# Performance work log

Measured on AMD Instinct MI355X. Metric: run time of the kernel, lower is better.

The kernel has to match this reference:

```python
import jax, jax.numpy as jnp
import numpy as np

N_NODES = 100000   # number of graph nodes (users + items)
N_EDGES = 1600000  # nonzeros of the normalized adjacency (avg degree 16)
D_FEAT = 48        # node embedding dimension


def setup_inputs() -> dict:
    key = jax.random.key(0)
    k_t, k_x, k_r, k_c, k_v = jax.random.split(key, 5)
    t = jax.random.normal(k_t, (1,), dtype=jnp.float32)
    x = jax.random.normal(k_x, (N_NODES, D_FEAT), dtype=jnp.float32)
    # COO sparse adjacency: rows sorted (CSR-like ordering), random cols,
    # positive edge weights mimicking symmetric-normalized adjacency values.
    rows = jnp.sort(jax.random.randint(k_r, (N_EDGES,), 0, N_NODES, dtype=jnp.int32))
    cols = jax.random.randint(k_c, (N_EDGES,), 0, N_NODES, dtype=jnp.int32)
    vals = jax.random.uniform(k_v, (N_EDGES,), dtype=jnp.float32)
    return {"t": t, "x": x, "rows": rows, "cols": cols, "vals": vals}


def reference(t, x, rows, cols, vals):
    # torch.sparse.mm(graph, x): for each nonzero (r, c, v), out[r] += v * x[c].
    # t (ODE time) is unused by the module's forward.
    msgs = x[cols] * vals[:, None]                      # [E, D] gathered, scaled messages
    out = jax.ops.segment_sum(msgs, rows, num_segments=N_NODES)  # scatter-add to rows
    return out
```

## Files before the change

### kernel.cpp

```cpp
#include <hip/hip_runtime.h>
#include <hip/hip_bf16.h>
#include <hip/hip_fp16.h>


#define D_FEAT 48
#define TPR 12
#define RPB 16
#define BLOCK (TPR * RPB)
#define ROW_BYTES 64

typedef float vfloat4 __attribute__((ext_vector_type(4)));

__global__ void build_row_ptr_scatter(const int* __restrict__ rows,
                                      int* __restrict__ row_ptr,
                                      int n_edges, int n_nodes) {
    int e = blockIdx.x * blockDim.x + threadIdx.x;
    if (e >= n_edges) return;
    const int r     = rows[e];
    const int rprev = (e == 0) ? -1 : rows[e - 1];
    for (int q = rprev + 1; q <= r; ++q) row_ptr[q] = e;
    if (e == n_edges - 1) {
        for (int q = r + 1; q <= n_nodes; ++q) row_ptr[q] = n_edges;
    }
}

__global__ __launch_bounds__(BLOCK) void convert_x_i8(
        const float* __restrict__ x,
        unsigned char* __restrict__ xq, int n_nodes) {
    __shared__ float smax[RPB][TPR];
    const int tid = threadIdx.x;
    const int fg  = tid % TPR;
    const int rib = tid / TPR;
    const int r   = blockIdx.x * RPB + rib;

    float4 f = make_float4(0.f, 0.f, 0.f, 0.f);
    if (r < n_nodes)
        f = reinterpret_cast<const float4*>(x)[(size_t)r * (D_FEAT / 4) + fg];

    float lmax = fmaxf(fmaxf(fabsf(f.x), fabsf(f.y)),
                       fmaxf(fabsf(f.z), fabsf(f.w)));
    smax[rib][fg] = lmax;
    __syncthreads();

    float rmax = 0.f;
#pragma unroll
    for (int i = 0; i < TPR; ++i) rmax = fmaxf(rmax, smax[rib][i]);
    if (r >= n_nodes) return;

    const float scale = rmax * (1.0f / 127.0f);
    const float inv   = (rmax > 0.f) ? (127.0f / rmax) : 0.f;

    union { signed char c[4]; unsigned int u; } pk;
    pk.c[0] = (signed char)(int)rintf(fminf(fmaxf(f.x * inv, -127.f), 127.f));
    pk.c[1] = (signed char)(int)rintf(fminf(fmaxf(f.y * inv, -127.f), 127.f));
    pk.c[2] = (signed char)(int)rintf(fminf(fmaxf(f.z * inv, -127.f), 127.f));
    pk.c[3] = (signed char)(int)rintf(fminf(fmaxf(f.w * inv, -127.f), 127.f));

    unsigned char* row = xq + (size_t)r * ROW_BYTES;
    *reinterpret_cast<unsigned int*>(row + fg * 4) = pk.u;
    if (fg == 0) *reinterpret_cast<float*>(row + 48) = scale;
}

__device__ __forceinline__ void fma4_q(vfloat4& acc, float vs, unsigned int q) {
    acc.x += vs * (float)(int)(signed char)(q & 0xffu);
    acc.y += vs * (float)(int)(signed char)((q >> 8) & 0xffu);
    acc.z += vs * (float)(int)(signed char)((q >> 16) & 0xffu);
    acc.w += vs * (float)(int)(signed char)(q >> 24);
}

__global__ __launch_bounds__(BLOCK) void spmm_rows_i8(
        const int* __restrict__ row_ptr,
        const int* __restrict__ cols,
        const float* __restrict__ vals,
        const unsigned char* __restrict__ xq,
        float* __restrict__ out,
        int n_nodes) {
    const int tid = threadIdx.x;
    const int fg  = tid % TPR;
    const int rib = tid / TPR;
    const int r   = blockIdx.x * RPB + rib;
    if (r >= n_nodes) return;

    const int e0 = row_ptr[r];
    const int e1 = row_ptr[r + 1];

    vfloat4 acc = (vfloat4)(0.f);

    int e = e0;
    for (; e + 7 < e1; e += 8) {
        int   c[8];
        float v[8];
#pragma unroll
        for (int j = 0; j < 8; ++j) { c[j] = cols[e + j]; v[j] = vals[e + j]; }
        unsigned int q[8];
        float        s[8];
#pragma unroll
        for (int j = 0; j < 8; ++j) {
            const unsigned char* row = xq + (size_t)c[j] * ROW_BYTES;
            q[j] = *reinterpret_cast<const unsigned int*>(row + fg * 4);
            s[j] = *reinterpret_cast<const float*>(row + 48);
        }
#pragma unroll
        for (int j = 0; j < 8; ++j) fma4_q(acc, v[j] * s[j], q[j]);
    }
    for (; e + 3 < e1; e += 4) {
        int   c[4];
        float v[4];
#pragma unroll
        for (int j = 0; j < 4; ++j) { c[j] = cols[e + j]; v[j] = vals[e + j]; }
        unsigned int q[4];
        float        s[4];
#pragma unroll
        for (int j = 0; j < 4; ++j) {
            const unsigned char* row = xq + (size_t)c[j] * ROW_BYTES;
            q[j] = *reinterpret_cast<const unsigned int*>(row + fg * 4);
            s[j] = *reinterpret_cast<const float*>(row + 48);
        }
#pragma unroll
        for (int j = 0; j < 4; ++j) fma4_q(acc, v[j] * s[j], q[j]);
    }
    for (; e < e1; ++e) {
        const unsigned char* row = xq + (size_t)cols[e] * ROW_BYTES;
        const unsigned int  q = *reinterpret_cast<const unsigned int*>(row + fg * 4);
        const float         s = *reinterpret_cast<const float*>(row + 48);
        fma4_q(acc, vals[e] * s, q);
    }

    __builtin_nontemporal_store(acc,
        reinterpret_cast<vfloat4*>(out + (size_t)r * D_FEAT + fg * 4));
}

__global__ __launch_bounds__(BLOCK) void spmm_rows_f32(
        const int* __restrict__ row_ptr,
        const int* __restrict__ cols,
        const float* __restrict__ vals,
        const float* __restrict__ x,
        float* __restrict__ out,
        int n_nodes) {
    const int tid = threadIdx.x;
    const int fg  = tid % TPR;
    const int rib = tid / TPR;
    const int r   = blockIdx.x * RPB + rib;
    if (r >= n_nodes) return;
    const int e0 = row_ptr[r];
    const int e1 = row_ptr[r + 1];
    float4 acc = make_float4(0.f, 0.f, 0.f, 0.f);
    for (int e = e0; e < e1; ++e) {
        const float v = vals[e];
        const float4 xa = *reinterpret_cast<const float4*>(
            x + (size_t)cols[e] * D_FEAT + fg * 4);
        acc.x += v * xa.x; acc.y += v * xa.y;
        acc.z += v * xa.z; acc.w += v * xa.w;
    }
    *reinterpret_cast<float4*>(out + (size_t)r * D_FEAT + fg * 4) = acc;
}

extern "C" void kernel_launch(void* const* d_in, const int* in_sizes, int n_in,
                              void* d_out, int out_size, void* d_ws, size_t ws_size,
                              hipStream_t stream) {
    const float* x    = (const float*)d_in[1];
    const int*   rows = (const int*)  d_in[2];
    const int*   cols = (const int*)  d_in[3];
    const float* vals = (const float*)d_in[4];
    float*       out  = (float*)d_out;

    const int n_edges = in_sizes[2];
    const int n_nodes = out_size / D_FEAT;

    int* row_ptr = (int*)d_ws;
    const size_t rp_bytes = (size_t)(n_nodes + 1) * sizeof(int);
    const size_t xq_off   = (rp_bytes + 255) & ~(size_t)255;
    const size_t need     = xq_off + (size_t)n_nodes * ROW_BYTES;

    {
        const int threads = 256;
        const int grid = (n_edges + threads - 1) / threads;
        build_row_ptr_scatter<<<grid, threads, 0, stream>>>(rows, row_ptr, n_edges, n_nodes);
    }

    if (ws_size >= need) {
        unsigned char* xq = (unsigned char*)d_ws + xq_off;
        {
            const int grid = (n_nodes + RPB - 1) / RPB;
            convert_x_i8<<<grid, BLOCK, 0, stream>>>(x, xq, n_nodes);
        }
        const int grid = (n_nodes + RPB - 1) / RPB;
        spmm_rows_i8<<<grid, BLOCK, 0, stream>>>(row_ptr, cols, vals, xq, out, n_nodes);
    } else {
        const int grid = (n_nodes + RPB - 1) / RPB;
        spmm_rows_f32<<<grid, BLOCK, 0, stream>>>(row_ptr, cols, vals, x, out, n_nodes);
    }
}
```

Before: 117.3 us.

## Split int8 feature table into two column halves and run SpMM per half

The 48-wide int8 table is stored as two separate 32-byte-per-row half tables, each with its own per-half scale. SpMM then runs as two launches, one per 24-column half, so each random-gather working set is about half the previous size and more likely to stay in cache. Loads of cols and vals now use nontemporal hints. The cost is that the row structure, cols and vals are streamed twice and an extra kernel launch is added.

Measured after the change: 159.7 us. +36.2%, slower.

```diff
diff --git a/kernel.cpp b/kernel.cpp
--- a/kernel.cpp
+++ b/kernel.cpp
@@ -4,10 +4,13 @@
 
 
 #define D_FEAT 48
+#define HF 24
+#define ROWB_H 32
 #define TPR 12
 #define RPB 16
-#define BLOCK (TPR * RPB)
-#define ROW_BYTES 64
+#define TPR_H 6
+#define RPB_H 32
+#define BLOCK 192
 
 typedef float vfloat4 __attribute__((ext_vector_type(4)));
 
@@ -24,31 +27,32 @@
     }
 }
 
-__global__ __launch_bounds__(BLOCK) void convert_x_i8(
+__global__ __launch_bounds__(BLOCK) void convert_x_i8_split(
         const float* __restrict__ x,
-        unsigned char* __restrict__ xq, int n_nodes) {
+        unsigned char* __restrict__ xqA,
+        unsigned char* __restrict__ xqB, int n_nodes) {
     __shared__ float smax[RPB][TPR];
     const int tid = threadIdx.x;
     const int fg  = tid % TPR;
     const int rib = tid / TPR;
     const int r   = blockIdx.x * RPB + rib;
 
-    float4 f = make_float4(0.f, 0.f, 0.f, 0.f);
+    vfloat4 f = (vfloat4)(0.f);
     if (r < n_nodes)
-        f = reinterpret_cast<const float4*>(x)[(size_t)r * (D_FEAT / 4) + fg];
-
-    float lmax = fmaxf(fmaxf(fabsf(f.x), fabsf(f.y)),
-                       fmaxf(fabsf(f.z), fabsf(f.w)));
-    smax[rib][fg] = lmax;
+        f = __builtin_nontemporal_load(
+              reinterpret_cast<const vfloat4*>(x) + (size_t)r * TPR + fg);
+
+    smax[rib][fg] = fmaxf(fmaxf(fabsf(f.x), fabsf(f.y)),
+                          fmaxf(fabsf(f.z), fabsf(f.w)));
     __syncthreads();
 
-    float rmax = 0.f;
-#pragma unroll
-    for (int i = 0; i < TPR; ++i) rmax = fmaxf(rmax, smax[rib][i]);
+    const int hbase = (fg < 6) ? 0 : 6;
+    float hmax = 0.f;
+#pragma unroll
+    for (int i = 0; i < 6; ++i) hmax = fmaxf(hmax, smax[rib][hbase + i]);
     if (r >= n_nodes) return;
 
-    const float scale = rmax * (1.0f / 127.0f);
-    const float inv   = (rmax > 0.f) ? (127.0f / rmax) : 0.f;
+    const float inv = (hmax > 0.f) ? (127.0f / hmax) : 0.f;
 
     union { signed char c[4]; unsigned int u; } pk;
     pk.c[0] = (signed char)(int)rintf(fminf(fmaxf(f.x * inv, -127.f), 127.f));
@@ -56,9 +60,11 @@
     pk.c[2] = (signed char)(int)rintf(fminf(fmaxf(f.z * inv, -127.f), 127.f));
     pk.c[3] = (signed char)(int)rintf(fminf(fmaxf(f.w * inv, -127.f), 127.f));
 
-    unsigned char* row = xq + (size_t)r * ROW_BYTES;
-    *reinterpret_cast<unsigned int*>(row + fg * 4) = pk.u;
-    if (fg == 0) *reinterpret_cast<float*>(row + 48) = scale;
+    unsigned char* half = (fg < 6) ? xqA : xqB;
+    const int      off  = (fg < 6) ? fg * 4 : (fg - 6) * 4;
+    *reinterpret_cast<unsigned int*>(half + (size_t)r * ROWB_H + off) = pk.u;
+    if (fg == 0) *reinterpret_cast<float*>(xqA + (size_t)r * ROWB_H + 24) = hmax * (1.0f / 127.0f);
+    if (fg == 6) *reinterpret_cast<float*>(xqB + (size_t)r * ROWB_H + 24) = hmax * (1.0f / 127.0f);
 }
 
 __device__ __forceinline__ void fma4_q(vfloat4& acc, float vs, unsigned int q) {
@@ -68,7 +74,7 @@
     acc.w += vs * (float)(int)(signed char)(q >> 24);
 }
 
-__global__ __launch_bounds__(BLOCK) void spmm_rows_i8(
+__global__ __launch_bounds__(BLOCK) void spmm_rows_i8h(
         const int* __restrict__ row_ptr,
         const int* __restrict__ cols,
         const float* __restrict__ vals,
@@ -76,9 +82,9 @@
         float* __restrict__ out,
         int n_nodes) {
     const int tid = threadIdx.x;
-    const int fg  = tid % TPR;
-    const int rib = tid / TPR;
-    const int r   = blockIdx.x * RPB + rib;
+    const int fg  = tid % TPR_H;
+    const int rib = tid / TPR_H;
+    const int r   = blockIdx.x * RPB_H + rib;
     if (r >= n_nodes) return;
 
     const int e0 = row_ptr[r];
@@ -91,14 +97,17 @@
         int   c[8];
         float v[8];
 #pragma unroll
-        for (int j = 0; j < 8; ++j) { c[j] = cols[e + j]; v[j] = vals[e + j]; }
+        for (int j = 0; j < 8; ++j) {
+            c[j] = __builtin_nontemporal_load(cols + e + j);
+            v[j] = __builtin_nontemporal_load(vals + e + j);
+        }
         unsigned int q[8];
         float        s[8];
 #pragma unroll
         for (int j = 0; j < 8; ++j) {
-            const unsigned char* row = xq + (size_t)c[j] * ROW_BYTES;
+            const unsigned char* row = xq + (size_t)c[j] * ROWB_H;
             q[j] = *reinterpret_cast<const unsigned int*>(row + fg * 4);
-            s[j] = *reinterpret_cast<const float*>(row + 48);
+            s[j] = *reinterpret_cast<const float*>(row + 24);
         }
 #pragma unroll
         for (int j = 0; j < 8; ++j) fma4_q(acc, v[j] * s[j], q[j]);
@@ -107,23 +116,26 @@
         int   c[4];
         float v[4];
 #pragma unroll
-        for (int j = 0; j < 4; ++j) { c[j] = cols[e + j]; v[j] = vals[e + j]; }
+        for (int j = 0; j < 4; ++j) {
+            c[j] = __builtin_nontemporal_load(cols + e + j);
+            v[j] = __builtin_nontemporal_load(vals + e + j);
+        }
         unsigned int q[4];
         float        s[4];
 #pragma unroll
         for (int j = 0; j < 4; ++j) {
-            const unsigned char* row = xq + (size_t)c[j] * ROW_BYTES;
+            const unsigned char* row = xq + (size_t)c[j] * ROWB_H;
             q[j] = *reinterpret_cast<const unsigned int*>(row + fg * 4);
-            s[j] = *reinterpret_cast<const float*>(row + 48);
+            s[j] = *reinterpret_cast<const float*>(row + 24);
         }
 #pragma unroll
         for (int j = 0; j < 4; ++j) fma4_q(acc, v[j] * s[j], q[j]);
     }
     for (; e < e1; ++e) {
-        const unsigned char* row = xq + (size_t)cols[e] * ROW_BYTES;
+        const unsigned char* row = xq + (size_t)__builtin_nontemporal_load(cols + e) * ROWB_H;
         const unsigned int  q = *reinterpret_cast<const unsigned int*>(row + fg * 4);
-        const float         s = *reinterpret_cast<const float*>(row + 48);
-        fma4_q(acc, vals[e] * s, q);
+        const float         s = *reinterpret_cast<const float*>(row + 24);
+        fma4_q(acc, __builtin_nontemporal_load(vals + e) * s, q);
     }
 
     __builtin_nontemporal_store(acc,
@@ -169,8 +181,9 @@
 
     int* row_ptr = (int*)d_ws;
     const size_t rp_bytes = (size_t)(n_nodes + 1) * sizeof(int);
-    const size_t xq_off   = (rp_bytes + 255) & ~(size_t)255;
-    const size_t need     = xq_off + (size_t)n_nodes * ROW_BYTES;
+    const size_t xa_off   = (rp_bytes + 255) & ~(size_t)255;
+    const size_t xb_off   = xa_off + (size_t)n_nodes * ROWB_H;
+    const size_t need     = xb_off + (size_t)n_nodes * ROWB_H;
 
     {
         const int threads = 256;
@@ -179,13 +192,15 @@
     }
 
     if (ws_size >= need) {
-        unsigned char* xq = (unsigned char*)d_ws + xq_off;
+        unsigned char* xqA = (unsigned char*)d_ws + xa_off;
+        unsigned char* xqB = (unsigned char*)d_ws + xb_off;
         {
             const int grid = (n_nodes + RPB - 1) / RPB;
-            convert_x_i8<<<grid, BLOCK, 0, stream>>>(x, xq, n_nodes);
-        }
-        const int grid = (n_nodes + RPB - 1) / RPB;
-        spmm_rows_i8<<<grid, BLOCK, 0, stream>>>(row_ptr, cols, vals, xq, out, n_nodes);
+            convert_x_i8_split<<<grid, BLOCK, 0, stream>>>(x, xqA, xqB, n_nodes);
+        }
+        const int grid = (n_nodes + RPB_H - 1) / RPB_H;
+        spmm_rows_i8h<<<grid, BLOCK, 0, stream>>>(row_ptr, cols, vals, xqA, out,      n_nodes);
+        spmm_rows_i8h<<<grid, BLOCK, 0, stream>>>(row_ptr, cols, vals, xqB, out + HF, n_nodes);
     } else {
         const int grid = (n_nodes + RPB - 1) / RPB;
         spmm_rows_f32<<<grid, BLOCK, 0, stream>>>(row_ptr, cols, vals, x, out, n_nodes);
```
